# Kernel tuning notes

Measured on AMD Instinct MI355X. Metric: run time of the kernel, lower is better.

Reference implementation:

```python
import jax, jax.numpy as jnp
import numpy as np
from jax import lax

B, P, GRID, NP = 16, 220, 4, 16
DIM, DEPTH, HEADS, DH, MLP, NC = 512, 6, 8, 64, 2048, 1000
EPS = 1e-5
SCALE = DH ** -0.5
FLAT = 64 * 16 * 16  # per-patch CNN output [64,16,16] flattened (c,p1,p2 order)


def setup_inputs() -> dict:
    key = jax.random.key(0)
    ks = iter(jax.random.split(key, 40))
    def n(shape, std):
        return jax.random.normal(next(ks), shape, dtype=jnp.float32) * std
    return {
        "img": jax.random.normal(next(ks), (B, 1, GRID * P, GRID * P), dtype=jnp.float32),
        "conv1_w": n((32, 1, 7, 7), (2.0 / 49) ** 0.5),
        "conv2_w": n((64, 32, 7, 7), (2.0 / (32 * 49)) ** 0.5),
        "conv3_w": n((64, 64, 7, 7), (2.0 / (64 * 49)) ** 0.5),
        "flat_w": n((FLAT, DIM), FLAT ** -0.5),
        "flat_b": jnp.zeros((DIM,), jnp.float32),
        "cls_token": n((1, 1, DIM), 0.02),
        "pos_emb": n((1, NP + 1, DIM), 0.02),
        "ln1_g": jnp.ones((DEPTH, DIM), jnp.float32),
        "ln1_b": jnp.zeros((DEPTH, DIM), jnp.float32),
        "qkv_w": n((DEPTH, DIM, 3 * HEADS * DH), DIM ** -0.5),
        "out_w": n((DEPTH, HEADS * DH, DIM), (HEADS * DH) ** -0.5),
        "out_b": jnp.zeros((DEPTH, DIM), jnp.float32),
        "ln2_g": jnp.ones((DEPTH, DIM), jnp.float32),
        "ln2_b": jnp.zeros((DEPTH, DIM), jnp.float32),
        "ff1_w": n((DEPTH, DIM, MLP), DIM ** -0.5),
        "ff1_b": jnp.zeros((DEPTH, MLP), jnp.float32),
        "ff2_w": n((DEPTH, MLP, DIM), MLP ** -0.5),
        "ff2_b": jnp.zeros((DEPTH, DIM), jnp.float32),
        "head_ln_g": jnp.ones((DIM,), jnp.float32),
        "head_ln_b": jnp.zeros((DIM,), jnp.float32),
        "head_w": n((DIM, NC), DIM ** -0.5),
        "head_b": jnp.zeros((NC,), jnp.float32),
    }


def _ln(x, g, b):
    m = jnp.mean(x, axis=-1, keepdims=True)
    v = jnp.mean(jnp.square(x - m), axis=-1, keepdims=True)
    return (x - m) * lax.rsqrt(v + EPS) * g + b


def _cnn(x, w1, w2, w3):
    def block(h, w):
        h = lax.conv_general_dilated(h, w, (2, 2), 'VALID',
                                     dimension_numbers=('NCHW', 'OIHW', 'NCHW'))
        h = jax.nn.relu(h)
        # MaxPool2d(kernel=7, stride=1, padding=1)
        return lax.reduce_window(h, -jnp.inf, lax.max, (1, 1, 7, 7), (1, 1, 1, 1),
                                 ((0, 0), (0, 0), (1, 1), (1, 1)))
    return block(block(block(x, w1), w2), w3)


def _forward(img, conv1_w, conv2_w, conv3_w, flat_w, flat_b, cls_token, pos_emb,
             ln1_g, ln1_b, qkv_w, out_w, out_b, ln2_g, ln2_b,
             ff1_w, ff1_b, ff2_w, ff2_b, head_ln_g, head_ln_b, head_w, head_b):
    # b c (h p1) (w p2) -> (b h w) 1 p1 p2 ; all patches batched through the CNN at once
    patches = img.reshape(B, 1, GRID, P, GRID, P).transpose(0, 2, 4, 3, 1, 5)
    patches = patches.reshape(B * NP, 1, P, P)
    feat = _cnn(patches, conv1_w, conv2_w, conv3_w).reshape(B, NP, FLAT)  # [B,NP,64*16*16]
    x = feat @ flat_w + flat_b                                            # [B,NP,DIM]
    x = jnp.concatenate([jnp.broadcast_to(cls_token, (B, 1, DIM)), x], axis=1) + pos_emb
    N = NP + 1

    def layer(x, p):
        g1, b1, qw, ow, ob, g2, b2, w1, fb1, w2, fb2 = p
        h = _ln(x, g1, b1)
        q, k, v = jnp.split(h @ qw, 3, axis=-1)
        def heads(t):
            return t.reshape(B, N, HEADS, DH).transpose(0, 2, 1, 3)  # b h n d
        q, k, v = heads(q), heads(k), heads(v)
        attn = jax.nn.softmax(jnp.einsum('bhqd,bhkd->bhqk', q, k) * SCALE, axis=-1)
        o = jnp.einsum('bhqk,bhkd->bhqd', attn, v).transpose(0, 2, 1, 3).reshape(B, N, HEADS * DH)
        x = x + o @ ow + ob
        h2 = _ln(x, g2, b2)
        x = x + jax.nn.gelu(h2 @ w1 + fb1, approximate=False) @ w2 + fb2
        return x, None

    x, _ = lax.scan(layer, x, (ln1_g, ln1_b, qkv_w, out_w, out_b,
                               ln2_g, ln2_b, ff1_w, ff1_b, ff2_w, ff2_b))
    cls = _ln(x[:, 0], head_ln_g, head_ln_b)
    return cls @ head_w + head_b  # [B, NC]


def reference(img, conv1_w, conv2_w, conv3_w, flat_w, flat_b, cls_token, pos_emb,
              ln1_g, ln1_b, qkv_w, out_w, out_b, ln2_g, ln2_b,
              ff1_w, ff1_b, ff2_w, ff2_b, head_ln_g, head_ln_b, head_w, head_b):
    return _forward(img, conv1_w, conv2_w, conv3_w, flat_w, flat_b, cls_token, pos_emb,
                    ln1_g, ln1_b, qkv_w, out_w, out_b, ln2_g, ln2_b,
                    ff1_w, ff1_b, ff2_w, ff2_b, head_ln_g, head_ln_b, head_w, head_b)
```

## Files before the change

kernel.cpp:

```cpp
#include <hip/hip_runtime.h>
#include <hip/hip_bf16.h>


typedef __hip_bfloat16 bf16;
typedef __attribute__((ext_vector_type(8))) short short8;
typedef __attribute__((ext_vector_type(4))) float floatx4;

#define CHUNK 64

union U8 { int4 v; unsigned short s[8]; };
__device__ inline void umax8(U8& a, const U8& b){
  #pragma unroll
  for (int j = 0; j < 8; j++) a.s[j] = (a.s[j] > b.s[j]) ? a.s[j] : b.s[j];
}
union U4 { uint2 v; unsigned short s[4]; };
__device__ inline void umax4(U4& a, const U4& b){
  #pragma unroll
  for (int j = 0; j < 4; j++) a.s[j] = (a.s[j] > b.s[j]) ? a.s[j] : b.s[j];
}

__global__ __launch_bounds__(256) void prep_w2(const float* __restrict__ w,
                                               bf16* __restrict__ w2b)
{
  int idx = blockIdx.x*256 + threadIdx.x;
  if (idx >= 49*64*32) return;
  int ic = idx & 31; int t = idx >> 5; int oc = t & 63; int kk = t >> 6;
  int ky = kk/7, kx = kk - ky*7;
  w2b[idx] = __float2bfloat16(w[((oc*32+ic)*7+ky)*7+kx]);
}

__global__ __launch_bounds__(256) void prep_w3(const float* __restrict__ w,
                                               bf16* __restrict__ w3b)
{
  int idx = blockIdx.x*256 + threadIdx.x;
  if (idx >= 49*2*64*32) return;
  int ic_l = idx & 31; int t = idx >> 5; int oc = t & 63; int t2 = t >> 6;
  int kx = t2 % 7; int t3 = t2 / 7; int kc = t3 & 1; int ky = t3 >> 1;
  w3b[idx] = __float2bfloat16(w[((oc*64 + kc*32 + ic_l)*7+ky)*7+kx]);
}

__global__ __launch_bounds__(256) void prep_pack(
    const float* __restrict__ src, bf16* __restrict__ dst,
    int K8, int N, int total)
{
  int idx = blockIdx.x*256 + threadIdx.x;
  if (idx >= total) return;
  int n = idx % N; int t = idx / N; int k8 = t % K8; int l = t / K8;
  const float* s = src + ((size_t)l*K8*8 + (size_t)k8*8)*N + n;
  union { bf16 h[8]; int4 v; } pk;
  #pragma unroll
  for (int j = 0; j < 8; j++) pk.h[j] = __float2bfloat16(s[(size_t)j*N]);
  *(int4*)(dst + (((size_t)l*K8 + k8)*N + n)*8) = pk.v;
}

__global__ __launch_bounds__(256) void prep_pack_flat(
    const float* __restrict__ src, bf16* __restrict__ hi, bf16* __restrict__ lo)
{
  int idx = blockIdx.x*256 + threadIdx.x;
  if (idx >= 2048*512) return;
  int n = idx & 511; int k8 = idx >> 9;
  const float* s = src + (size_t)k8*8*512 + n;
  union { bf16 h[8]; int4 v; } ph, pl;
  #pragma unroll
  for (int j = 0; j < 8; j++){
    float w = s[(size_t)j*512];
    bf16 h = __float2bfloat16(w);
    ph.h[j] = h;
    pl.h[j] = __float2bfloat16(w - __bfloat162float(h));
  }
  size_t o = (size_t)idx*8;
  *(int4*)(hi + o) = ph.v;
  *(int4*)(lo + o) = pl.v;
}

__global__ __launch_bounds__(256) void k1a_conv1(
    const float* __restrict__ img, const float* __restrict__ w,
    bf16* __restrict__ cbuf, int n_base)
{
  __shared__ __align__(16) float in_s[15*224];
  __shared__ float w_s[32*58];
  const int band = blockIdx.x;
  const int n = blockIdx.y;
  const int ng = n_base + n;
  const int r0 = band*5;
  const int ir0 = 2*r0;
  const int b = ng>>4, gh = (ng>>2)&3, gw = ng&3;
  const float* ibase = img + b*774400 + (gh*220)*880 + gw*220;

  for (int idx = threadIdx.x; idx < 15*56; idx += 256){
    int r = idx/56, cq = idx - r*56; int c = cq*4;
    int gr = ir0 + r;
    float4 v = (c < 220 && gr < 220) ? *(const float4*)(ibase + gr*880 + c)
                                     : make_float4(0.f,0.f,0.f,0.f);
    *(float4*)&in_s[r*224 + c] = v;
  }
  for (int idx = threadIdx.x; idx < 32*56; idx += 256){
    int oc = idx/56, k = idx - oc*56; int ky = k>>3, kx = k&7;
    w_s[oc*58 + k] = (kx < 7) ? w[oc*49 + ky*7 + kx] : 0.f;
  }
  __syncthreads();

  const int grp = threadIdx.x & 7;
  const int sp  = threadIdx.x >> 3;
  const int cgc = (sp < 26) ? sp : 26;
  const int nrows = (107 - r0 < 5) ? (107 - r0) : 5;

  float acc[5][4][4] = {};
  #pragma unroll 1
  for (int ky = 0; ky < 7; ky++){
    float wk[4][7];
    #pragma unroll
    for (int oc = 0; oc < 4; oc++)
      #pragma unroll
      for (int kx = 0; kx < 7; kx++)
        wk[oc][kx] = w_s[(grp*4+oc)*58 + ky*8 + kx];
    #pragma unroll
    for (int i = 0; i < 5; i++){
      if (i < nrows){
        const float* ip = &in_s[(2*i+ky)*224 + 8*cgc];
        float iv[13];
        *(float4*)&iv[0] = *(const float4*)ip;
        *(float4*)&iv[4] = *(const float4*)(ip+4);
        *(float4*)&iv[8] = *(const float4*)(ip+8);
        iv[12] = ip[12];
        #pragma unroll
        for (int oc = 0; oc < 4; oc++)
          #pragma unroll
          for (int kx = 0; kx < 7; kx++)
            #pragma unroll
            for (int j = 0; j < 4; j++)
              acc[i][oc][j] += iv[2*j+kx]*wk[oc][kx];
      }
    }
  }

  #pragma unroll
  for (int i = 0; i < 5; i++){
    if (i < nrows){
      int y = r0 + i;
      #pragma unroll
      for (int j = 0; j < 4; j++){
        int col = 4*sp + j;
        if (col < 107){
          union { unsigned short s[4]; uint2 u; } pk;
          #pragma unroll
          for (int oc = 0; oc < 4; oc++){
            bf16 hv = __float2bfloat16(fmaxf(acc[i][oc][j], 0.f));
            pk.s[oc] = *(unsigned short*)&hv;
          }
          *(uint2*)(cbuf + (((size_t)(n*8+grp)*107 + y)*107 + col)*4) = pk.u;
        }
      }
    }
  }
}

__global__ __launch_bounds__(256) void k1b_pool1(
    const bf16* __restrict__ cbuf, bf16* __restrict__ pool1, int n_pool_base)
{
  __shared__ uint2 in4[19*107];
  __shared__ uint2 ht4[19*103];
  const int s = blockIdx.x, g = blockIdx.y, n = blockIdx.z;
  const int p0 = s*13;
  const int PR = (103 - p0 < 13) ? (103 - p0) : 13;
  const int NR = PR + 6;
  const uint2* src = (const uint2*)cbuf + (size_t)(n*8+g)*107*107;

  for (int t = threadIdx.x; t < NR*107; t += 256){
    int r = t/107, c = t - r*107;
    int gr = p0 - 1 + r;
    gr = (gr < 0) ? 0 : ((gr > 106) ? 106 : gr);
    in4[t] = src[gr*107 + c];
  }
  __syncthreads();
  for (int t = threadIdx.x; t < NR*103; t += 256){
    int r = t/103, c = t - r*103;
    U4 m; m.v = in4[r*107 + ((c > 0) ? c-1 : 0)];
    #pragma unroll
    for (int d = 0; d < 6; d++){
      U4 v; v.v = in4[r*107 + ((c+d < 106) ? c+d : 106)];
      umax4(m, v);
    }
    ht4[r*103 + c] = m.v;
  }
  __syncthreads();
  uint2* dst = (uint2*)pool1 + (size_t)((n_pool_base + n)*8 + g)*10609;
  for (int t = threadIdx.x; t < PR*103; t += 256){
    int pr = t/103, c = t - pr*103;
    U4 m; m.v = ht4[pr*103 + c];
    #pragma unroll
    for (int d = 1; d < 7; d++){
      U4 v; v.v = ht4[(pr+d)*103 + c];
      umax4(m, v);
    }
    dst[(p0+pr)*103 + c] = m.v;
  }
}

__global__ __launch_bounds__(256) void k2_conv2(
    const bf16* __restrict__ pool1,
    const bf16* __restrict__ w2b,
    bf16* __restrict__ conv2out)
{
  __shared__ __align__(16) bf16 in_s[7*2*52*40];
  const int n = blockIdx.y, pb = blockIdx.x;
  const int wv = threadIdx.x >> 6, lane = threadIdx.x & 63;
  const int li = lane & 15, lg = lane >> 4;
  const int p0 = pb*256;
  const int y0 = p0/49;

  int pyv[4], pxv[4], poff[4]; bool pmask[4];
  #pragma unroll
  for (int t = 0; t < 4; t++){
    int p = p0 + wv*64 + t*16 + li;
    pmask[t] = (p <= 2400);
    int pc = min(p, 2400);
    int yy = pc/49, xx = pc - yy*49;
    pyv[t] = yy; pxv[t] = xx;
    poff[t] = ((yy - y0)*2*52 + xx)*40;
  }
  floatx4 acc[4][4];
  #pragma unroll
  for (int a = 0; a < 4; a++)
    #pragma unroll
    for (int t = 0; t < 4; t++) acc[a][t] = (floatx4){0.f,0.f,0.f,0.f};

  const unsigned short* pbase = (const unsigned short*)pool1;
  for (int ky = 0; ky < 7; ky++){
    __syncthreads();
    for (int idx = threadIdx.x; idx < 7*103*4; idx += 256){
      int q = idx & 3; int t2 = idx >> 2; int c = t2 % 103; int r = t2/103;
      int gr = min(2*(y0+r)+ky, 102);
      size_t pix = (size_t)gr*103 + c;
      uint2 lov = *(const uint2*)(pbase + (((size_t)n*8 + 2*q  )*10609 + pix)*4);
      uint2 hiv = *(const uint2*)(pbase + (((size_t)n*8 + 2*q+1)*10609 + pix)*4);
      int4 vv; vv.x = (int)lov.x; vv.y = (int)lov.y; vv.z = (int)hiv.x; vv.w = (int)hiv.y;
      *(int4*)&in_s[((r*2 + (c&1))*52 + (c>>1))*40 + q*8] = vv;
    }
    __syncthreads();
    #pragma unroll
    for (int kx = 0; kx < 7; kx++){
      short8 a[4];
      const bf16* wp = w2b + (ky*7+kx)*64*32;
      #pragma unroll
      for (int ot = 0; ot < 4; ot++)
        a[ot] = *(const short8*)(wp + (ot*16 + li)*32 + lg*8);
      int koff = ((kx&1)*52 + (kx>>1))*40 + lg*8;
      #pragma unroll
      for (int t = 0; t < 4; t++){
        short8 bfr = *(const short8*)(&in_s[poff[t] + koff]);
        #pragma unroll
        for (int ot = 0; ot < 4; ot++)
          acc[ot][t] = __builtin_amdgcn_mfma_f32_16x16x32_bf16(a[ot], bfr, acc[ot][t], 0, 0, 0);
      }
    }
  }
  #pragma unroll
  for (int t = 0; t < 4; t++){
    if (!pmask[t]) continue;
    bf16* dst = conv2out + (((long)n*49 + pyv[t])*49 + pxv[t])*64 + lg*4;
    #pragma unroll
    for (int ot = 0; ot < 4; ot++){
      union { bf16 h[4]; uint2 u; } pk;
      #pragma unroll
      for (int v = 0; v < 4; v++)
        pk.h[v] = __float2bfloat16(fmaxf(acc[ot][t][v], 0.f));
      *(uint2*)(dst + ot*16) = pk.u;
    }
  }
}

__global__ __launch_bounds__(256) void k3a_hmax(
    const bf16* __restrict__ cin, bf16* __restrict__ tmp)
{
  int idx = blockIdx.x*256 + threadIdx.x;
  int cg = idx & 7; int t = idx >> 3; int x = t % 45; int t2 = t / 45;
  int y = t2 % 49; int n = t2 / 49;
  const int4* row = (const int4*)(cin + ((long)(n*49 + y)*49)*64) + cg;
  U8 m; m.v = make_int4(0,0,0,0);
  int lo = max(x-1, 0), hi = min(x+5, 48);
  for (int cx = lo; cx <= hi; cx++){ U8 v; v.v = row[cx*8]; umax8(m, v); }
  *((int4*)(tmp + ((long)(n*49 + y)*45 + x)*64) + cg) = m.v;
}

__global__ __launch_bounds__(256) void k3b_vmax(
    const bf16* __restrict__ tmp, bf16* __restrict__ pout, int n_base)
{
  int idx = blockIdx.x*256 + threadIdx.x;
  int cg = idx & 7; int t = idx >> 3; int x = t % 45; int t2 = t / 45;
  int y = t2 % 45; int n = t2 / 45;
  U8 m; m.v = make_int4(0,0,0,0);
  int lo = max(y-1, 0), hi = min(y+5, 48);
  for (int cy = lo; cy <= hi; cy++){
    U8 v; v.v = *((const int4*)(tmp + ((long)(n*49 + cy)*45 + x)*64) + cg);
    umax8(m, v);
  }
  *((int4*)(pout + (long)(n_base+n)*129600 + (y*45 + x)*64) + cg) = m.v;
}

__global__ __launch_bounds__(256) void k4_conv3(
    const bf16* __restrict__ pool2,
    const bf16* __restrict__ w3b,
    bf16* __restrict__ conv3out)
{
  __shared__ __align__(16) bf16 in_s[10*2*24*40];
  const int n = blockIdx.y, pb = blockIdx.x;
  const int wv = threadIdx.x >> 6, lane = threadIdx.x & 63;
  const int li = lane & 15, lg = lane >> 4;
  const int y0 = pb*10;

  int pyv[4], pxv[4], poff[4]; bool pmask[4];
  #pragma unroll
  for (int t = 0; t < 4; t++){
    int pl = wv*64 + t*16 + li;
    pmask[t] = (pl < 200);
    int p = pb*200 + min(pl, 199);
    int yy = p/20, xx = p - yy*20;
    pyv[t] = yy; pxv[t] = xx;
    poff[t] = ((yy - y0)*2*24 + xx)*40;
  }
  floatx4 acc[4][4];
  #pragma unroll
  for (int a = 0; a < 4; a++)
    #pragma unroll
    for (int t = 0; t < 4; t++) acc[a][t] = (floatx4){0.f,0.f,0.f,0.f};

  for (int ky = 0; ky < 7; ky++){
    for (int kc = 0; kc < 2; kc++){
      __syncthreads();
      for (int idx = threadIdx.x; idx < 10*45*4; idx += 256){
        int q = idx & 3; int t2 = idx >> 2; int c = t2 % 45; int r = t2/45;
        int gr = 2*(y0+r)+ky;
        const bf16* src = pool2 + (((long)n*45 + gr)*45 + c)*64 + kc*32 + q*8;
        bf16* dst = &in_s[((r*2 + (c&1))*24 + (c>>1))*40 + q*8];
        *(int4*)dst = *(const int4*)src;
      }
      __syncthreads();
      #pragma unroll
      for (int kx = 0; kx < 7; kx++){
        short8 a[4];
        const bf16* wp = w3b + ((ky*2+kc)*7 + kx)*64*32;
        #pragma unroll
        for (int ot = 0; ot < 4; ot++)
          a[ot] = *(const short8*)(wp + (ot*16 + li)*32 + lg*8);
        int koff = ((kx&1)*24 + (kx>>1))*40 + lg*8;
        #pragma unroll
        for (int t = 0; t < 4; t++){
          short8 bfr = *(const short8*)(&in_s[poff[t] + koff]);
          #pragma unroll
          for (int ot = 0; ot < 4; ot++)
            acc[ot][t] = __builtin_amdgcn_mfma_f32_16x16x32_bf16(a[ot], bfr, acc[ot][t], 0, 0, 0);
        }
      }
    }
  }
  #pragma unroll
  for (int t = 0; t < 4; t++){
    if (!pmask[t]) continue;
    bf16* dst = conv3out + (((long)n*20 + pyv[t])*20 + pxv[t])*64 + lg*4;
    #pragma unroll
    for (int ot = 0; ot < 4; ot++){
      union { bf16 h[4]; uint2 u; } pk;
      #pragma unroll
      for (int v = 0; v < 4; v++)
        pk.h[v] = __float2bfloat16(fmaxf(acc[ot][t][v], 0.f));
      *(uint2*)(dst + ot*16) = pk.u;
    }
  }
}

__global__ __launch_bounds__(256) void k5_pool3(
    const bf16* __restrict__ cin, bf16* __restrict__ feat)
{
  __shared__ int4 in_p[3200];
  __shared__ int4 ht[2560];
  const int n = blockIdx.x;
  const int4* src = (const int4*)(cin + (long)n*25600);
  for (int i = threadIdx.x; i < 3200; i += 256) in_p[i] = src[i];
  __syncthreads();
  for (int i = threadIdx.x; i < 2560; i += 256){
    int cg = i & 7; int t = i >> 3; int x = t & 15; int y = t >> 4;
    U8 m; m.v = make_int4(0,0,0,0);
    int lo = max(x-1, 0), hi = min(x+5, 19);
    for (int cx = lo; cx <= hi; cx++){ U8 v; v.v = in_p[(y*20+cx)*8 + cg]; umax8(m, v); }
    ht[(y*16+x)*8 + cg] = m.v;
  }
  __syncthreads();
  unsigned short* dst = (unsigned short*)(feat + (long)n*16384);
  for (int i = threadIdx.x; i < 2048; i += 256){
    int px = i & 15; int py = (i >> 4) & 15; int cg = i >> 8;
    U8 m; m.v = make_int4(0,0,0,0);
    int lo = max(py-1, 0), hi = min(py+5, 19);
    for (int cy = lo; cy <= hi; cy++){ U8 v; v.v = ht[(cy*16+px)*8 + cg]; umax8(m, v); }
    #pragma unroll
    for (int j = 0; j < 8; j++)
      dst[(cg*8+j)*256 + py*16 + px] = m.s[j];
  }
}

__global__ __launch_bounds__(256) void k6_init_x(
    const float* __restrict__ cls, const float* __restrict__ pos,
    const float* __restrict__ flat_b, float* __restrict__ x)
{
  int idx = blockIdx.x*256 + threadIdx.x;
  int d = idx & 511; int row = idx >> 9;
  int tt = row % 17;
  x[idx] = (tt == 0) ? (cls[d] + pos[d]) : (flat_b[d] + pos[tt*512 + d]);
}

__global__ __launch_bounds__(256) void k6_flat_mfma(
    const bf16* __restrict__ feat, const bf16* __restrict__ Whi,
    const bf16* __restrict__ Wlo, float* __restrict__ x)
{
  const int wv = threadIdx.x >> 6, lane = threadIdx.x & 63;
  const int li = lane & 15, lg = lane >> 4;
  const int m0 = blockIdx.x*64 + wv*16;
  const int nb = blockIdx.y*64;
  const int kb = blockIdx.z*2048;
  floatx4 acc[4];
  #pragma unroll
  for (int t = 0; t < 4; t++) acc[t] = (floatx4){0.f,0.f,0.f,0.f};

  const bf16* arow = feat + (size_t)(m0+li)*16384 + kb + lg*8;
  for (int k0 = 0; k0 < 2048; k0 += 32){
    short8 a = *(const short8*)(arow + k0);
    size_t wo = ((size_t)((kb + k0) >> 3) + lg)*512 + nb + li;
    const bf16* wh = Whi + wo*8;
    const bf16* wl = Wlo + wo*8;
    #pragma unroll
    for (int t = 0; t < 4; t++){
      short8 bh = *(const short8*)(wh + t*128);
      acc[t] = __builtin_amdgcn_mfma_f32_16x16x32_bf16(a, bh, acc[t], 0, 0, 0);
    }
    #pragma unroll
    for (int t = 0; t < 4; t++){
      short8 bl = *(const short8*)(wl + t*128);
      acc[t] = __builtin_amdgcn_mfma_f32_16x16x32_bf16(a, bl, acc[t], 0, 0, 0);
    }
  }
  #pragma unroll
  for (int t = 0; t < 4; t++){
    int col = nb + t*16 + li;
    #pragma unroll
    for (int v = 0; v < 4; v++){
      int m = m0 + lg*4 + v;
      int row = (m>>4)*17 + 1 + (m&15);
      atomicAdd(&x[row*512 + col], acc[t][v]);
    }
  }
}

__global__ __launch_bounds__(256) void ln_kernel(
    const float* __restrict__ in, const float* __restrict__ g,
    const float* __restrict__ b, float* __restrict__ out,
    int in_stride, int out_stride)
{
  int row = blockIdx.x;
  const float* p = in + (long)row*in_stride;
  float v0 = p[threadIdx.x], v1 = p[threadIdx.x+256];
  __shared__ float red[4]; __shared__ float stat;
  float s = v0+v1;
  #pragma unroll
  for (int o = 32; o >= 1; o >>= 1) s += __shfl_down(s, o);
  int lane = threadIdx.x & 63, wv = threadIdx.x >> 6;
  if (lane == 0) red[wv] = s;
  __syncthreads();
  if (threadIdx.x == 0) stat = (red[0]+red[1]+red[2]+red[3])*(1.0f/512.0f);
  __syncthreads();
  float m = stat;
  float d0 = v0-m, d1 = v1-m;
  float q = d0*d0 + d1*d1;
  #pragma unroll
  for (int o = 32; o >= 1; o >>= 1) q += __shfl_down(q, o);
  __syncthreads();
  if (lane == 0) red[wv] = q;
  __syncthreads();
  if (threadIdx.x == 0) stat = rsqrtf((red[0]+red[1]+red[2]+red[3])*(1.0f/512.0f) + 1e-5f);
  __syncthreads();
  float rstd = stat;
  out[(long)row*out_stride + threadIdx.x]     = d0*rstd*g[threadIdx.x]     + b[threadIdx.x];
  out[(long)row*out_stride + threadIdx.x+256] = d1*rstd*g[threadIdx.x+256] + b[threadIdx.x+256];
}

__global__ __launch_bounds__(256) void ln_bf16(
    const float* __restrict__ in, const float* __restrict__ g,
    const float* __restrict__ b, bf16* __restrict__ out)
{
  int row = blockIdx.x;
  const float* p = in + (long)row*512;
  float v0 = p[threadIdx.x], v1 = p[threadIdx.x+256];
  __shared__ float red[4]; __shared__ float stat;
  float s = v0+v1;
  #pragma unroll
  for (int o = 32; o >= 1; o >>= 1) s += __shfl_down(s, o);
  int lane = threadIdx.x & 63, wv = threadIdx.x >> 6;
  if (lane == 0) red[wv] = s;
  __syncthreads();
  if (threadIdx.x == 0) stat = (red[0]+red[1]+red[2]+red[3])*(1.0f/512.0f);
  __syncthreads();
  float m = stat;
  float d0 = v0-m, d1 = v1-m;
  float q = d0*d0 + d1*d1;
  #pragma unroll
  for (int o = 32; o >= 1; o >>= 1) q += __shfl_down(q, o);
  __syncthreads();
  if (lane == 0) red[wv] = q;
  __syncthreads();
  if (threadIdx.x == 0) stat = rsqrtf((red[0]+red[1]+red[2]+red[3])*(1.0f/512.0f) + 1e-5f);
  __syncthreads();
  float rstd = stat;
  out[(long)row*512 + threadIdx.x]     = __float2bfloat16(d0*rstd*g[threadIdx.x]     + b[threadIdx.x]);
  out[(long)row*512 + threadIdx.x+256] = __float2bfloat16(d1*rstd*g[threadIdx.x+256] + b[threadIdx.x+256]);
}

template<int NT>
__global__ __launch_bounds__(256) void tail_gemm(
    const bf16* __restrict__ A, const bf16* __restrict__ Wp,
    const float* __restrict__ bias, const float* res,
    float* outf, bf16* outb, int N, int K, int dogelu)
{
  const int wv = threadIdx.x >> 6, lane = threadIdx.x & 63;
  const int li = lane & 15, lg = lane >> 4;
  const int m0 = blockIdx.x * 16;
  const int nb = blockIdx.y * (64*NT) + wv * (16*NT);
  floatx4 acc[NT];
  #pragma unroll
  for (int t = 0; t < NT; t++) acc[t] = (floatx4){0.f,0.f,0.f,0.f};
  const bf16* arow = A + (size_t)(m0+li)*K + lg*8;
  for (int k0 = 0; k0 < K; k0 += 32){
    short8 a = *(const short8*)(arow + k0);
    const bf16* wrow = Wp + ((size_t)((k0>>3) + lg) * N + nb + li) * 8;
    #pragma unroll
    for (int t = 0; t < NT; t++){
      short8 bfr = *(const short8*)(wrow + t*128);
      acc[t] = __builtin_amdgcn_mfma_f32_16x16x32_bf16(a, bfr, acc[t], 0, 0, 0);
    }
  }
  #pragma unroll
  for (int t = 0; t < NT; t++){
    int col = nb + t*16 + li;
    #pragma unroll
    for (int v = 0; v < 4; v++){
      int row = m0 + lg*4 + v;
      float val = acc[t][v];
      if (bias) val += bias[col];
      if (dogelu) val = 0.5f*val*(1.0f + erff(val*0.70710678118654752f));
      if (res) val += res[(size_t)row*N + col];
      if (outf) outf[(size_t)row*N + col] = val;
      else      outb[(size_t)row*N + col] = __float2bfloat16(val);
    }
  }
}

__global__ __launch_bounds__(256) void gemm_rows(
    const float* __restrict__ A, const float* __restrict__ W,
    const float* __restrict__ bias, const float* __restrict__ res,
    float* __restrict__ out, int M, int N, int K, int dogelu)
{
  __shared__ float A_s[16][33];
  __shared__ __align__(16) float W_s[32][68];
  const int m0 = blockIdx.x*16, n0 = blockIdx.y*64;
  const int r = threadIdx.x>>4, c0 = (threadIdx.x&15)*4;
  float acc[4] = {};
  for (int k0 = 0; k0 < K; k0 += 32){
    __syncthreads();
    for (int i = 0; i < 2; i++){ int id = threadIdx.x + i*256; int rr = id>>5, kk = id&31;
      A_s[rr][kk] = (m0+rr < M) ? A[(long)(m0+rr)*K + k0+kk] : 0.f; }
    for (int i = 0; i < 8; i++){ int id = threadIdx.x + i*256; int kk = id>>6, c = id&63;
      W_s[kk][c] = (n0+c < N) ? W[(long)(k0+kk)*N + n0+c] : 0.f; }
    __syncthreads();
    #pragma unroll
    for (int kk = 0; kk < 32; kk++){
      float a = A_s[r][kk];
      float4 w4 = *(const float4*)&W_s[kk][c0];
      acc[0]+=a*w4.x; acc[1]+=a*w4.y; acc[2]+=a*w4.z; acc[3]+=a*w4.w;
    }
  }
  if (m0+r < M){
    int row = m0+r;
    for (int j = 0; j < 4; j++){
      int c = n0+c0+j;
      if (c < N){
        float v = acc[j];
        if (bias) v += bias[c];
        if (dogelu) v = 0.5f*v*(1.0f + erff(v*0.70710678118654752f));
        if (res) v += res[(long)row*N + c];
        out[(long)row*N + c] = v;
      }
    }
  }
}

__global__ __launch_bounds__(128) void attn_kernel(
    const float* __restrict__ qkv, bf16* __restrict__ obuf)
{
  const int b = blockIdx.x >> 3, h = blockIdx.x & 7;
  __shared__ float q_s[17][65], k_s[17][65], v_s[17][65], s_s[17][18];
  for (int idx = threadIdx.x; idx < 17*64; idx += 128){
    int i = idx>>6, d = idx&63;
    const float* base = qkv + (long)(b*17+i)*1536 + h*64 + d;
    q_s[i][d] = base[0]; k_s[i][d] = base[512]; v_s[i][d] = base[1024];
  }
  __syncthreads();
  for (int idx = threadIdx.x; idx < 289; idx += 128){
    int i = idx/17, j = idx - i*17;
    float s = 0.f;
    for (int d = 0; d < 64; d++) s += q_s[i][d]*k_s[j][d];
    s_s[i][j] = s*0.125f;
  }
  __syncthreads();
  if (threadIdx.x < 17){
    int i = threadIdx.x;
    float m = -1e30f;
    for (int j = 0; j < 17; j++) m = fmaxf(m, s_s[i][j]);
    float sum = 0.f;
    for (int j = 0; j < 17; j++){ float e = expf(s_s[i][j]-m); s_s[i][j] = e; sum += e; }
    float inv = 1.0f/sum;
    for (int j = 0; j < 17; j++) s_s[i][j] *= inv;
  }
  __syncthreads();
  for (int idx = threadIdx.x; idx < 17*64; idx += 128){
    int i = idx>>6, d = idx&63;
    float o = 0.f;
    for (int j = 0; j < 17; j++) o += s_s[i][j]*v_s[j][d];
    obuf[(long)(b*17+i)*512 + h*64 + d] = __float2bfloat16(o);
  }
}

extern "C" void kernel_launch(void* const* d_in, const int* in_sizes, int n_in,
                              void* d_out, int out_size, void* d_ws, size_t ws_size,
                              hipStream_t stream) {
  const float* img      = (const float*)d_in[0];
  const float* conv1_w  = (const float*)d_in[1];
  const float* conv2_w  = (const float*)d_in[2];
  const float* conv3_w  = (const float*)d_in[3];
  const float* flat_w   = (const float*)d_in[4];
  const float* flat_b   = (const float*)d_in[5];
  const float* cls_tok  = (const float*)d_in[6];
  const float* pos_emb  = (const float*)d_in[7];
  const float* ln1_g    = (const float*)d_in[8];
  const float* ln1_b    = (const float*)d_in[9];
  const float* qkv_w    = (const float*)d_in[10];
  const float* out_w    = (const float*)d_in[11];
  const float* out_b    = (const float*)d_in[12];
  const float* ln2_g    = (const float*)d_in[13];
  const float* ln2_b    = (const float*)d_in[14];
  const float* ff1_w    = (const float*)d_in[15];
  const float* ff1_b    = (const float*)d_in[16];
  const float* ff2_w    = (const float*)d_in[17];
  const float* ff2_b    = (const float*)d_in[18];
  const float* hln_g    = (const float*)d_in[19];
  const float* hln_b    = (const float*)d_in[20];
  const float* head_w   = (const float*)d_in[21];
  const float* head_b   = (const float*)d_in[22];

  char* ws = (char*)d_ws;
  size_t off = 0;
  auto alloc = [&](size_t bytes) -> void* {
    void* p = ws + off; off += (bytes + 255) & ~(size_t)255; return p;
  };
  bf16* pool1    = (bf16*)alloc((size_t)CHUNK*8*103*103*4*2);
  bf16* conv2out = (bf16*)alloc((size_t)CHUNK*49*49*64*2);
  bf16* pool2    = (bf16*)alloc((size_t)256*45*45*64*2);
  bf16* feat     = (bf16*)alloc((size_t)256*16384*2);
  bf16* w2b      = (bf16*)alloc((size_t)49*64*32*2);
  bf16* w3b      = (bf16*)alloc((size_t)49*2*64*32*2);
  float* x       = (float*)alloc((size_t)139264*4);
  bf16*  hb      = (bf16*)alloc((size_t)139264*2);
  float* qkvb    = (float*)alloc((size_t)417792*4);
  bf16*  obufb   = (bf16*)alloc((size_t)139264*2);
  bf16*  ffbufb  = (bf16*)alloc((size_t)557056*2);
  float* hcls    = (float*)alloc((size_t)8192*4);
  bf16* tmp3     = pool1;
  bf16* conv3out = pool1;
  bf16* qkvp  = pool1;
  bf16* outwp = qkvp  + (size_t)6*512*1536;
  bf16* ff1p  = outwp + (size_t)6*512*512;
  bf16* ff2p  = ff1p  + (size_t)6*512*2048;
  bf16* fwhi  = conv2out;
  bf16* fwlo  = pool2;

  const size_t cb_per_n = (size_t)8*107*107*4*2;
  int SUB; bf16* cbuf;
  if (ws_size >= off + 64*cb_per_n)      { SUB = 64; cbuf = (bf16*)alloc(64*cb_per_n); }
  else if (ws_size >= off + 32*cb_per_n) { SUB = 32; cbuf = (bf16*)alloc(32*cb_per_n); }
  else { SUB = 16; cbuf = conv2out; }
  (void)in_sizes; (void)n_in; (void)out_size;

  prep_w2<<<392, 256, 0, stream>>>(conv2_w, w2b);
  prep_w3<<<784, 256, 0, stream>>>(conv3_w, w3b);

  for (int cb = 0; cb < 256; cb += CHUNK){
    for (int sb = 0; sb < CHUNK; sb += SUB){
      k1a_conv1<<<dim3(22, SUB), 256, 0, stream>>>(img, conv1_w, cbuf, cb + sb);
      k1b_pool1<<<dim3(8, 8, SUB), 256, 0, stream>>>(cbuf, pool1, sb);
    }
    k2_conv2     <<<dim3(10,CHUNK), 256, 0, stream>>>(pool1, w2b, conv2out);
    k3a_hmax     <<<(CHUNK*49*45*8)/256, 256, 0, stream>>>(conv2out, tmp3);
    k3b_vmax     <<<(CHUNK*45*45*8)/256, 256, 0, stream>>>(tmp3, pool2, cb);
  }
  k4_conv3<<<dim3(2,256), 256, 0, stream>>>(pool2, w3b, conv3out);
  k5_pool3<<<256, 256, 0, stream>>>(conv3out, feat);

  prep_pack_flat<<<4096, 256, 0, stream>>>(flat_w, fwhi, fwlo);
  prep_pack<<<(6*64*1536+255)/256, 256, 0, stream>>>(qkv_w, qkvp, 64, 1536, 6*64*1536);
  prep_pack<<<(6*64*512 +255)/256, 256, 0, stream>>>(out_w, outwp, 64, 512,  6*64*512);
  prep_pack<<<(6*64*2048+255)/256, 256, 0, stream>>>(ff1_w, ff1p, 64, 2048, 6*64*2048);
  prep_pack<<<(6*256*512+255)/256, 256, 0, stream>>>(ff2_w, ff2p, 256, 512, 6*256*512);

  k6_init_x    <<<544,         256, 0, stream>>>(cls_tok, pos_emb, flat_b, x);
  k6_flat_mfma <<<dim3(4,8,8), 256, 0, stream>>>(feat, fwhi, fwlo, x);

  for (int l = 0; l < 6; l++){
    ln_bf16<<<272, 256, 0, stream>>>(x, ln1_g + l*512, ln1_b + l*512, hb);
    tail_gemm<4><<<dim3(17,6), 256, 0, stream>>>(hb, qkvp + (size_t)l*786432,
                                                 nullptr, nullptr, qkvb, nullptr, 1536, 512, 0);
    attn_kernel<<<128, 128, 0, stream>>>(qkvb, obufb);
    tail_gemm<1><<<dim3(17,8), 256, 0, stream>>>(obufb, outwp + (size_t)l*262144,
                                                 out_b + l*512, x, x, nullptr, 512, 512, 0);
    ln_bf16<<<272, 256, 0, stream>>>(x, ln2_g + l*512, ln2_b + l*512, hb);
    tail_gemm<4><<<dim3(17,8), 256, 0, stream>>>(hb, ff1p + (size_t)l*1048576,
                                                 ff1_b + l*2048, nullptr, nullptr, ffbufb, 2048, 512, 1);
    tail_gemm<1><<<dim3(17,8), 256, 0, stream>>>(ffbufb, ff2p + (size_t)l*1048576,
                                                 ff2_b + l*512, x, x, nullptr, 512, 2048, 0);
  }

  ln_kernel<<<16, 256, 0, stream>>>(x, hln_g, hln_b, hcls, 17*512, 512);
  gemm_rows<<<dim3(1,16), 256, 0, stream>>>(hcls, head_w, head_b, nullptr,
                                            (float*)d_out, 16, 1000, 512, 0);
}
```

Before: 1.720 ms.

## Register-prefetch conv2/conv3 input tiles and interleave pool1 channel layout

The pool1 output layout now interleaves pairs of 4-channel groups, so conv2 can fetch eight channels with a single 16-byte load instead of two 8-byte loads. Conv2 and conv3 now load the next ky (or ky/kc) input slab into registers while the current slab is used by MFMA, then write it to shared memory at the next phase. This hides global load latency behind compute, at the cost of more registers (12 or 8 int4 per thread), which may lower occupancy.

Result: slower. 1.897 ms (+10.3%).

```diff
diff --git a/kernel.cpp b/kernel.cpp
--- a/kernel.cpp
+++ b/kernel.cpp
@@ -184,7 +184,9 @@
     ht4[r*103 + c] = m.v;
   }
   __syncthreads();
-  uint2* dst = (uint2*)pool1 + (size_t)((n_pool_base + n)*8 + g)*10609;
+  uint2* dst = (uint2*)pool1;
+  const size_t plane = ((size_t)(n_pool_base + n)*4 + (g>>1))*10609;
+  const int h = g & 1;
   for (int t = threadIdx.x; t < PR*103; t += 256){
     int pr = t/103, c = t - pr*103;
     U4 m; m.v = ht4[pr*103 + c];
@@ -193,7 +195,7 @@
       U4 v; v.v = ht4[(pr+d)*103 + c];
       umax4(m, v);
     }
-    dst[(p0+pr)*103 + c] = m.v;
+    dst[(plane + (size_t)(p0+pr)*103 + c)*2 + h] = m.v;
   }
 }
 
@@ -226,17 +228,35 @@
     for (int t = 0; t < 4; t++) acc[a][t] = (floatx4){0.f,0.f,0.f,0.f};
 
   const unsigned short* pbase = (const unsigned short*)pool1;
+  int4 pre[12];
+
+  auto stage_load = [&](int ky){
+    #pragma unroll
+    for (int i = 0; i < 12; i++){
+      int idx = threadIdx.x + i*256;
+      if (idx < 7*103*4){
+        int q = idx & 3; int t2 = idx >> 2; int c = t2 % 103; int r = t2/103;
+        int gr = min(2*(y0+r)+ky, 102);
+        pre[i] = *(const int4*)(pbase + (((size_t)n*4 + q)*10609 + (size_t)gr*103 + c)*8);
+      }
+    }
+  };
+  auto stage_write = [&](){
+    #pragma unroll
+    for (int i = 0; i < 12; i++){
+      int idx = threadIdx.x + i*256;
+      if (idx < 7*103*4){
+        int q = idx & 3; int t2 = idx >> 2; int c = t2 % 103; int r = t2/103;
+        *(int4*)&in_s[((r*2 + (c&1))*52 + (c>>1))*40 + q*8] = pre[i];
+      }
+    }
+  };
+
+  stage_load(0);
   for (int ky = 0; ky < 7; ky++){
     __syncthreads();
-    for (int idx = threadIdx.x; idx < 7*103*4; idx += 256){
-      int q = idx & 3; int t2 = idx >> 2; int c = t2 % 103; int r = t2/103;
-      int gr = min(2*(y0+r)+ky, 102);
-      size_t pix = (size_t)gr*103 + c;
-      uint2 lov = *(const uint2*)(pbase + (((size_t)n*8 + 2*q  )*10609 + pix)*4);
-      uint2 hiv = *(const uint2*)(pbase + (((size_t)n*8 + 2*q+1)*10609 + pix)*4);
-      int4 vv; vv.x = (int)lov.x; vv.y = (int)lov.y; vv.z = (int)hiv.x; vv.w = (int)hiv.y;
-      *(int4*)&in_s[((r*2 + (c&1))*52 + (c>>1))*40 + q*8] = vv;
-    }
+    stage_write();
+    if (ky < 6) stage_load(ky+1);
     __syncthreads();
     #pragma unroll
     for (int kx = 0; kx < 7; kx++){
@@ -325,32 +345,50 @@
     #pragma unroll
     for (int t = 0; t < 4; t++) acc[a][t] = (floatx4){0.f,0.f,0.f,0.f};
 
-  for (int ky = 0; ky < 7; ky++){
-    for (int kc = 0; kc < 2; kc++){
-      __syncthreads();
-      for (int idx = threadIdx.x; idx < 10*45*4; idx += 256){
+  int4 pre[8];
+  auto stage_load = [&](int ph){
+    int ky = ph >> 1, kc = ph & 1;
+    #pragma unroll
+    for (int i = 0; i < 8; i++){
+      int idx = threadIdx.x + i*256;
+      if (idx < 10*45*4){
         int q = idx & 3; int t2 = idx >> 2; int c = t2 % 45; int r = t2/45;
         int gr = 2*(y0+r)+ky;
-        const bf16* src = pool2 + (((long)n*45 + gr)*45 + c)*64 + kc*32 + q*8;
-        bf16* dst = &in_s[((r*2 + (c&1))*24 + (c>>1))*40 + q*8];
-        *(int4*)dst = *(const int4*)src;
-      }
-      __syncthreads();
+        pre[i] = *(const int4*)(pool2 + (((long)n*45 + gr)*45 + c)*64 + kc*32 + q*8);
+      }
+    }
+  };
+  auto stage_write = [&](){
+    #pragma unroll
+    for (int i = 0; i < 8; i++){
+      int idx = threadIdx.x + i*256;
+      if (idx < 10*45*4){
+        int q = idx & 3; int t2 = idx >> 2; int c = t2 % 45; int r = t2/45;
+        *(int4*)&in_s[((r*2 + (c&1))*24 + (c>>1))*40 + q*8] = pre[i];
+      }
+    }
+  };
+
+  stage_load(0);
+  for (int ph = 0; ph < 14; ph++){
+    __syncthreads();
+    stage_write();
+    if (ph < 13) stage_load(ph+1);
+    __syncthreads();
+    #pragma unroll
+    for (int kx = 0; kx < 7; kx++){
+      short8 a[4];
+      const bf16* wp = w3b + (ph*7 + kx)*64*32;
       #pragma unroll
-      for (int kx = 0; kx < 7; kx++){
-        short8 a[4];
-        const bf16* wp = w3b + ((ky*2+kc)*7 + kx)*64*32;
+      for (int ot = 0; ot < 4; ot++)
+        a[ot] = *(const short8*)(wp + (ot*16 + li)*32 + lg*8);
+      int koff = ((kx&1)*24 + (kx>>1))*40 + lg*8;
+      #pragma unroll
+      for (int t = 0; t < 4; t++){
+        short8 bfr = *(const short8*)(&in_s[poff[t] + koff]);
         #pragma unroll
         for (int ot = 0; ot < 4; ot++)
-          a[ot] = *(const short8*)(wp + (ot*16 + li)*32 + lg*8);
-        int koff = ((kx&1)*24 + (kx>>1))*40 + lg*8;
-        #pragma unroll
-        for (int t = 0; t < 4; t++){
-          short8 bfr = *(const short8*)(&in_s[poff[t] + koff]);
-          #pragma unroll
-          for (int ot = 0; ot < 4; ot++)
-            acc[ot][t] = __builtin_amdgcn_mfma_f32_16x16x32_bf16(a[ot], bfr, acc[ot][t], 0, 0, 0);
-        }
+          acc[ot][t] = __builtin_amdgcn_mfma_f32_16x16x32_bf16(a[ot], bfr, acc[ot][t], 0, 0, 0);
       }
     }
   }
```
